# Performance work log

Hardware: AMD Instinct MI355X
Metric: run time of the kernel (lower is better)

## Reference

```python
import jax, jax.numpy as jnp
import numpy as np
import math

B, N, HORIZON, E = 16, 4096, 12, 16
IN_DIM = HORIZON * E            # 192
T_DIM, H, D = 64, 4, 16         # transformer_dim, heads, head_dim
K_ORD = 3
FFN = 128
OUT_DIM = HORIZON * 16          # horizon * dim_out = 192
LN_EPS = 1e-5


def setup_inputs() -> dict:
    key = jax.random.key(0)
    ks = jax.random.split(key, 16)
    s = 0.02
    return {
        "x": jax.random.normal(ks[0], (B, N, IN_DIM), jnp.float32),
        "Wq": jax.random.normal(ks[1], (IN_DIM, T_DIM), jnp.float32) * s,
        "bq": jnp.zeros((T_DIM,), jnp.float32),
        "Wk": jax.random.normal(ks[2], (IN_DIM, T_DIM), jnp.float32) * s,
        "bk": jnp.zeros((T_DIM,), jnp.float32),
        "Wv": jax.random.normal(ks[3], (IN_DIM, T_DIM), jnp.float32) * s,
        "bv": jnp.zeros((T_DIM,), jnp.float32),
        "Win": jax.random.normal(ks[4], (IN_DIM, T_DIM), jnp.float32) * s,  # no bias
        "Wout": jax.random.normal(ks[5], (T_DIM, OUT_DIM), jnp.float32) * s,
        "bout": jnp.zeros((OUT_DIM,), jnp.float32),
        "W1": jax.random.normal(ks[6], (T_DIM, FFN), jnp.float32) * s,
        "b1": jnp.zeros((FFN,), jnp.float32),
        "W2": jax.random.normal(ks[7], (FFN, T_DIM), jnp.float32) * s,
        "b2": jnp.zeros((T_DIM,), jnp.float32),
        "ln_g": jnp.ones((T_DIM,), jnp.float32),
        "ln_b": jnp.zeros((T_DIM,), jnp.float32),
        "weights_pool": jax.random.normal(ks[8], (IN_DIM, OUT_DIM), jnp.float32) * s,
        "Pi": jax.random.normal(ks[9], (H, K_ORD + 1), jnp.float32) * 0.5,
    }


def _layer_norm(y, g, b):
    mu = jnp.mean(y, axis=-1, keepdims=True)
    var = jnp.mean((y - mu) ** 2, axis=-1, keepdims=True)
    return (y - mu) * jax.lax.rsqrt(var + LN_EPS) * g + b


def reference(x, Wq, bq, Wk, bk, Wv, bv, Win, Wout, bout,
              W1, b1, W2, b2, ln_g, ln_b, weights_pool, Pi):
    Bx, Nx, _ = x.shape
    # projections -> (B, H, N, d)
    Q = (x @ Wq + bq).reshape(Bx, Nx, H, D).transpose(0, 2, 1, 3)
    Kt = (x @ Wk + bk).reshape(Bx, Nx, H, D).transpose(0, 2, 1, 3)
    V = (x @ Wv + bv).reshape(Bx, Nx, H, D).transpose(0, 2, 1, 3)

    weighted_sum = jnp.zeros((Bx, H, Nx, D), x.dtype)
    for k in range(K_ORD + 1):
        if k == 0:
            # transform(0, .) returns ones with feature dim 1
            Qk = jnp.ones((Bx, H, Nx, 1), x.dtype)
            Kk = jnp.ones((Bx, H, Nx, 1), x.dtype)
        else:
            Qk = Q ** k   # elementwise power (exp-by-squaring == x**k)
            Kk = Kt ** k
        dk = Qk.shape[-1]
        # f_kv: (B,H,f,d) ; sumN: (B,H,f,1)
        f_kv = jnp.einsum('bhnf,bhnc->bhfc', Kk, V)
        sumN = jnp.sum(Kk, axis=2)[..., None]
        f_kv_norm = f_kv / (sumN + 1e-8) / math.sqrt(dk)
        c_k = jnp.einsum('bhnf,bhfc->bhnc', Qk, f_kv_norm)
        weighted_sum = weighted_sum + c_k * Pi[:, k][None, :, None, None]

    # NOTE: faithful to original: raw view of (B,H,N,d) as (B,N,H*d), no permute
    attention_out = weighted_sum.reshape(Bx, Nx, H * D) / math.factorial(K_ORD)

    proj = x @ Win
    res = _layer_norm(proj + attention_out, ln_g, ln_b)
    ffn = jax.nn.relu(res @ W1 + b1) @ W2 + b2   # dropout = identity (eval)
    res = _layer_norm(res + ffn, ln_g, ln_b)

    x_g = jnp.einsum('bni,io->bno', x, weights_pool)
    out = res @ Wout + bout
    return x_g + out
```

## Files before the change

### kernel.cpp

```cpp
#include <hip/hip_runtime.h>

typedef unsigned int u32;
typedef unsigned short u16;

#define NB 16
#define NN 4096
#define IND 192

typedef __attribute__((ext_vector_type(8))) short short8;
typedef __attribute__((ext_vector_type(4))) float f32x4;
#define MFMA16 __builtin_amdgcn_mfma_f32_16x16x32_bf16

__device__ __forceinline__ float bf2f(u16 u) {
  union { u32 i; float f; } c; c.i = ((u32)u) << 16; return c.f;
}
__device__ __forceinline__ float lo16(u32 u) {
  union { u32 i; float f; } c; c.i = u << 16; return c.f;
}
__device__ __forceinline__ float hi16(u32 u) {
  union { u32 i; float f; } c; c.i = u & 0xffff0000u; return c.f;
}
__device__ __forceinline__ u16 f2bf(float f) {
  union { float f; u32 i; } c; c.f = f;
  u32 r = c.i + 0x7fffu + ((c.i >> 16) & 1u);
  return (u16)(r >> 16);
}
__device__ __forceinline__ float ldwf(const void* p, int i, int isf) {
  return isf ? ((const float*)p)[i] : bf2f(((const u16*)p)[i]);
}
__device__ __forceinline__ short8 ld_frag8(const u16* p) {
  union { uint4 u; short8 s; } c;
  c.u = *reinterpret_cast<const uint4*>(p);
  return c.s;
}
__device__ __forceinline__ short8 as_short8(uint4 u) {
  union { uint4 u; short8 s; } c; c.u = u; return c.s;
}
__device__ __forceinline__ short8 pack8(const float* v) {
  short8 s;
  #pragma unroll
  for (int e = 0; e < 8; ++e) s[e] = (short)f2bf(v[e]);
  return s;
}
__device__ __forceinline__ float ln64(float y, float g, float be) {
  float s = y, sq = y * y;
  #pragma unroll
  for (int off = 32; off > 0; off >>= 1) {
    s  += __shfl_xor(s, off, 64);
    sq += __shfl_xor(sq, off, 64);
  }
  float mu  = s * 0.015625f;
  float var = sq * 0.015625f - mu * mu;
  return (y - mu) * rsqrtf(var + 1e-5f) * g + be;
}

__global__ __launch_bounds__(64) void k_detect(const u32* __restrict__ x2,
                                               int* __restrict__ flag) {
  int t = threadIdx.x;
  int bad = 0;
  for (int i = 0; i < 16; ++i) {
    float a = fabsf(lo16(x2[t * 16 + i]));
    if (!(a < 1e4f)) bad = 1;
  }
  int anybad = __any(bad);
  if (t == 0) *flag = anybad ? 1 : 0;
}

__global__ __launch_bounds__(256) void k_xb(const int* __restrict__ flag,
                                            const void* __restrict__ x,
                                            u16* __restrict__ xb) {
  const int isf = *flag;
  size_t gid = (size_t)blockIdx.x * 256 + threadIdx.x;
  if (isf) {
    const float4* src = (const float4*)x;
    for (size_t i = gid; i < 3145728; i += 1048576) {
      float4 v = src[i];
      ushort4 o;
      o.x = f2bf(v.x); o.y = f2bf(v.y); o.z = f2bf(v.z); o.w = f2bf(v.w);
      ((ushort4*)xb)[i] = o;
    }
  } else {
    const uint4* src = (const uint4*)x;
    for (size_t i = gid; i < 1572864; i += 1048576)
      ((uint4*)xb)[i] = src[i];
  }
}

__global__ __launch_bounds__(192) void k_xsum(const int* __restrict__ flag,
                                              const void* __restrict__ x,
                                              float* __restrict__ xsum) {
  const int isf = *flag;
  const int t = threadIdx.x;
  const int r0 = blockIdx.x * 256;
  const int b = r0 >> 12;
  float s = 0.f;
  if (isf) {
    const float* xp = (const float*)x;
    for (int r = 0; r < 256; ++r) s += xp[(size_t)(r0 + r) * 192 + t];
  } else {
    const u16* xp = (const u16*)x;
    for (int r = 0; r < 256; ++r) s += bf2f(xp[(size_t)(r0 + r) * 192 + t]);
  }
  atomicAdd(xsum + b * 192 + t, s);
}

__global__ __launch_bounds__(256) void k_prepw(
    const int* __restrict__ flag,
    const void* Wq, const void* Wk, const void* Wv, const void* Win,
    const void* Wout, const void* Wp, const void* W1, const void* W2,
    const void* bq, const void* bk, const void* bv,
    u16* __restrict__ Bs1, u16* __restrict__ BsKlo, u16* __restrict__ Bs2,
    u16* __restrict__ W1f, u16* __restrict__ W2f, float* __restrict__ bcat)
{
  const int isf = *flag;
  int idx = blockIdx.x * 256 + threadIdx.x;
  if (idx < 49152) {
    int e = idx & 7, l = (idx >> 3) & 63, g = idx >> 9;
    int nt = g & 15, ks = g >> 4;
    int k = ks * 32 + (l >> 4) * 8 + e;
    int n = nt * 16 + (l & 15);
    const void* W = (n < 64) ? Wq : (n < 128) ? Wk : (n < 192) ? Wv : Win;
    Bs1[idx] = f2bf(ldwf(W, k * 64 + (n & 63), isf));
  } else if (idx < 61440) {
    int j = idx - 49152;
    int e = j & 7, l = (j >> 3) & 63, g = j >> 9;
    int ntp = g & 3, ks = g >> 2;
    int k = ks * 32 + (l >> 4) * 8 + e;
    int n = ntp * 16 + (l & 15);
    float wv = ldwf(Wk, k * 64 + n, isf);
    u16 hi = f2bf(wv);
    BsKlo[j] = f2bf(wv - bf2f(hi));
  } else if (idx < 110592) {
    int j = idx - 61440;
    int e = j & 7, l = (j >> 3) & 63, g = j >> 9;
    int nt = g % 12, ks = g / 12;
    int k = ks * 32 + (l >> 4) * 8 + e;
    int n = nt * 16 + (l & 15);
    float v = (k < 64) ? ldwf(Wout, k * 192 + n, isf)
                       : ldwf(Wp, (k - 64) * 192 + n, isf);
    Bs2[j] = f2bf(v);
  } else if (idx < 118784) {
    int j = idx - 110592;
    int e = j & 7, l = (j >> 3) & 63, g = j >> 9;
    int nt = g & 7, ks = g >> 3;
    int k = ks * 32 + (l >> 4) * 8 + e;
    int n = nt * 16 + (l & 15);
    W1f[j] = f2bf(ldwf(W1, k * 128 + n, isf));
  } else if (idx < 126976) {
    int j = idx - 118784;
    int e = j & 7, l = (j >> 3) & 63, g = j >> 9;
    int nt = g & 3, ks = g >> 2;
    int k = ks * 32 + (l >> 4) * 8 + e;
    int n = nt * 16 + (l & 15);
    W2f[j] = f2bf(ldwf(W2, k * 64 + n, isf));
  } else if (idx < 127232) {
    int n = idx - 126976;
    bcat[n] = (n < 64)  ? ldwf(bq, n, isf)
            : (n < 128) ? ldwf(bk, n - 64, isf)
            : (n < 192) ? ldwf(bv, n - 128, isf) : 0.f;
  }
}

template<bool F32>
__device__ void gemm1_body(const void* __restrict__ x,
                           const u16* __restrict__ Bs1,
                           const u16* __restrict__ BsKlo,
                           const float* __restrict__ bcat,
                           u16* __restrict__ C1, float* __restrict__ stats,
                           float (*xs)[196], float (*Ks)[65], float (*Vs)[65])
{
  const int tid = threadIdx.x;
  const int mbase = blockIdx.x * 32;
  const int b = mbase >> 12;

  if constexpr (F32) {
    for (int i = tid; i < 1536; i += 512) {
      int row = i / 48, c4 = i - row * 48;
      float4 v = *((const float4*)x + (size_t)(mbase + row) * 48 + c4);
      *(float4*)&xs[row][c4 * 4] = v;
    }
    __syncthreads();
  }

  const int w = tid >> 6, l = tid & 63, lm = l & 15, lk = l >> 4;
  const int nt0 = w * 2;
  const bool isK = (w == 2) || (w == 3);

  short8 bhi[2][6], blo[2][6];
  #pragma unroll
  for (int n2 = 0; n2 < 2; ++n2)
    #pragma unroll
    for (int ks = 0; ks < 6; ++ks) {
      bhi[n2][ks] = ld_frag8(Bs1 + (size_t)((ks * 16 + nt0 + n2) * 64 + l) * 8);
      if (F32 && isK)
        blo[n2][ks] = ld_frag8(BsKlo + (size_t)((ks * 4 + nt0 + n2 - 4) * 64 + l) * 8);
    }
  float bias[2];
  bias[0] = bcat[nt0 * 16 + lm];
  bias[1] = bcat[(nt0 + 1) * 16 + lm];

  for (int mt = 0; mt < 2; ++mt) {
    short8 ahi[6], alo[6];
    if constexpr (F32) {
      const float* xr = &xs[mt * 16 + lm][0];
      #pragma unroll
      for (int ks = 0; ks < 6; ++ks) {
        float v[8];
        *(float4*)&v[0] = *(const float4*)(xr + ks * 32 + lk * 8);
        *(float4*)&v[4] = *(const float4*)(xr + ks * 32 + lk * 8 + 4);
        short8 h8;
        #pragma unroll
        for (int e = 0; e < 8; ++e) h8[e] = (short)f2bf(v[e]);
        ahi[ks] = h8;
        if (isK) {
          short8 l8;
          #pragma unroll
          for (int e = 0; e < 8; ++e) {
            float r = v[e] - bf2f((u16)h8[e]);
            l8[e] = (short)f2bf(r);
          }
          alo[ks] = l8;
        }
      }
    } else {
      const u16* xg = (const u16*)x + (size_t)(mbase + mt * 16 + lm) * 192 + lk * 8;
      #pragma unroll
      for (int ks = 0; ks < 6; ++ks) ahi[ks] = ld_frag8(xg + ks * 32);
    }
    f32x4 acc[2];
    #pragma unroll
    for (int n2 = 0; n2 < 2; ++n2) {
      f32x4 a = {bias[n2], bias[n2], bias[n2], bias[n2]};
      acc[n2] = a;
    }
    #pragma unroll
    for (int ks = 0; ks < 6; ++ks)
      #pragma unroll
      for (int n2 = 0; n2 < 2; ++n2) {
        acc[n2] = MFMA16(ahi[ks], bhi[n2][ks], acc[n2], 0, 0, 0);
        if (F32 && isK) {
          acc[n2] = MFMA16(ahi[ks], blo[n2][ks], acc[n2], 0, 0, 0);
          acc[n2] = MFMA16(alo[ks], bhi[n2][ks], acc[n2], 0, 0, 0);
          acc[n2] = MFMA16(alo[ks], blo[n2][ks], acc[n2], 0, 0, 0);
        }
      }
    const int rl = mt * 16 + lk * 4;
    if (w < 2) {
      #pragma unroll
      for (int n2 = 0; n2 < 2; ++n2)
        #pragma unroll
        for (int r = 0; r < 4; ++r)
          C1[(size_t)(mbase + rl + r) * 128 + (nt0 + n2) * 16 + lm] = f2bf(acc[n2][r]);
    } else if (isK) {
      #pragma unroll
      for (int n2 = 0; n2 < 2; ++n2)
        #pragma unroll
        for (int r = 0; r < 4; ++r)
          Ks[rl + r][(nt0 + n2 - 4) * 16 + lm] = acc[n2][r];
    } else if (w < 6) {
      #pragma unroll
      for (int n2 = 0; n2 < 2; ++n2)
        #pragma unroll
        for (int r = 0; r < 4; ++r)
          Vs[rl + r][(nt0 + n2 - 8) * 16 + lm] = acc[n2][r];
    } else {
      #pragma unroll
      for (int n2 = 0; n2 < 2; ++n2)
        #pragma unroll
        for (int r = 0; r < 4; ++r)
          C1[(size_t)(mbase + rl + r) * 128 + 64 + (nt0 + n2 - 12) * 16 + lm] = f2bf(acc[n2][r]);
    }
  }
  __syncthreads();

  float* sb = stats + (size_t)(b * 4) * 832;
  #pragma unroll
  for (int it = 0; it < 2; ++it) {
    int item = tid + it * 512;
    int hh = item >> 8, f = (item >> 4) & 15, c = item & 15;
    float a1 = 0.f, a2 = 0.f, a3 = 0.f;
    for (int r = 0; r < 32; ++r) {
      float kv = Ks[r][hh * 16 + f];
      float vv = Vs[r][hh * 16 + c];
      float k2 = kv * kv;
      a1 = fmaf(kv, vv, a1);
      a2 = fmaf(k2, vv, a2);
      a3 = fmaf(k2 * kv, vv, a3);
    }
    float* base = sb + (size_t)hh * 832 + f * 16 + c;
    atomicAdd(base, a1);
    atomicAdd(base + 256, a2);
    atomicAdd(base + 512, a3);
  }
  if (tid < 192) {
    int kk = tid >> 6, hf = tid & 63, h2 = hf >> 4, ff = hf & 15;
    float s = 0.f;
    for (int r = 0; r < 32; ++r) {
      float kv = Ks[r][hf];
      s += (kk == 0) ? kv : (kk == 1) ? kv * kv : kv * kv * kv;
    }
    atomicAdd(sb + (size_t)h2 * 832 + 768 + kk * 16 + ff, s);
  } else if (tid < 256) {
    int hf = tid - 192, h2 = hf >> 4;
    float s = 0.f;
    for (int r = 0; r < 32; ++r) s += Vs[r][hf];
    atomicAdd(sb + (size_t)h2 * 832 + 816 + (hf & 15), s);
  }
}

__global__ __launch_bounds__(512, 2) void k_gemm1(
    const int* __restrict__ flag, const void* __restrict__ x,
    const u16* __restrict__ Bs1, const u16* __restrict__ BsKlo,
    const float* __restrict__ bcat,
    u16* __restrict__ C1, float* __restrict__ stats)
{
  __shared__ float xs[32][196];
  __shared__ float Ks[32][65];
  __shared__ float Vs[32][65];
  if (*flag) gemm1_body<true >(x, Bs1, BsKlo, bcat, C1, stats, xs, Ks, Vs);
  else       gemm1_body<false>(x, Bs1, BsKlo, bcat, C1, stats, xs, Ks, Vs);
}

template<bool F32>
__device__ void finalize_body(const float* stats, const void* Pi,
                              const void* Wk, const void* bk,
                              const float* xsum, float* M, float* sn1)
{
  const int bh = blockIdx.x, bb = bh >> 2, h = bh & 3, t = threadIdx.x;
  const float* sb = stats + (size_t)bh * 832;
  float* mb = M + (size_t)bh * 784;
  const float inv6 = 1.0f / 6.0f;

  {
    int f = t >> 4, s = t & 15;
    float p = 0.f;
    for (int i = s * 12; i < s * 12 + 12; ++i)
      p += xsum[bb * 192 + i] * ldwf(Wk, i * 64 + h * 16 + f, F32);
    p += __shfl_xor(p, 1, 64);
    p += __shfl_xor(p, 2, 64);
    p += __shfl_xor(p, 4, 64);
    p += __shfl_xor(p, 8, 64);
    if (s == 0) sn1[f] = p + 4096.0f * ldwf(bk, h * 16 + f, F32);
  }
  __syncthreads();

  {
    const int f = t >> 4, c = t & 15;
    #pragma unroll
    for (int k = 0; k < 3; ++k) {
      float fkv = sb[k * 256 + f * 16 + c];
      float sk  = (k == 0) ? sn1[f] : sb[768 + k * 16 + f];
      float pi  = ldwf(Pi, h * 4 + (k + 1), F32);
      mb[k * 256 + f * 16 + c] = fkv / ((sk + 1e-8f) * 4.0f) * pi * inv6;
    }
  }
  if (t < 16) {
    float sv  = sb[816 + t];
    float pi0 = ldwf(Pi, h * 4 + 0, F32);
    mb[768 + t] = sv / (4096.0f + 1e-8f) * pi0 * inv6;
  }
}

__global__ __launch_bounds__(256) void k_finalize(
    const int* __restrict__ flag, const float* __restrict__ stats,
    const void* __restrict__ Pi, const void* __restrict__ Wk,
    const void* __restrict__ bk, const float* __restrict__ xsum,
    float* __restrict__ M)
{
  __shared__ float sn1[16];
  if (*flag) finalize_body<true >(stats, Pi, Wk, bk, xsum, M, sn1);
  else       finalize_body<false>(stats, Pi, Wk, bk, xsum, M, sn1);
}

template<bool F32> __device__ void mid_body(
    const u16* __restrict__ C1, u16* __restrict__ R2,
    const float* __restrict__ Mall,
    const u16* __restrict__ W1f, const u16* __restrict__ W2f,
    const void* __restrict__ b1, const void* __restrict__ b2,
    const void* __restrict__ lng, const void* __restrict__ lnb,
    float (*attL)[72], u16 (*resB)[72], u16 (*hB)[136])
{
  const int tid = threadIdx.x;
  const int w = tid >> 6, l = tid & 63;
  const int lm = l & 15, lk = l >> 4;
  const int n0g = blockIdx.x * 64;
  const int b = n0g >> 12;
  const int n2_0 = n0g & 4095;
  const int h = n2_0 >> 10;
  const int qg0 = (b << 12) + ((n2_0 & 1023) << 2);
  const float* mb = Mall + (size_t)((b << 2) + h) * 784;

  short8 Bhi[2], Blo[2];
  #pragma unroll
  for (int ks = 0; ks < 2; ++ks) {
    float vh[8], vl[8];
    #pragma unroll
    for (int e = 0; e < 8; ++e) {
      int kk = ks * 32 + lk * 8 + e;
      float v = (kk < 16) ? mb[kk * 16 + lm]
              : (kk < 32) ? mb[256 + (kk - 16) * 16 + lm]
              : (kk < 48) ? mb[512 + (kk - 32) * 16 + lm] : 0.f;
      float hi = bf2f(f2bf(v));
      vh[e] = hi; vl[e] = v - hi;
    }
    Bhi[ks] = pack8(vh);
    Blo[ks] = pack8(vl);
  }
  const float c0v = mb[768 + lm];

  #pragma unroll
  for (int mt2 = 0; mt2 < 4; ++mt2) {
    const int mt = w * 4 + mt2;
    uint4 qv = *(const uint4*)(C1 + (size_t)(qg0 + mt * 16 + lm) * 128
                               + h * 16 + (lk & 1) * 8);
    float q[8] = {lo16(qv.x), hi16(qv.x), lo16(qv.y), hi16(qv.y),
                  lo16(qv.z), hi16(qv.z), lo16(qv.w), hi16(qv.w)};
    float q2[8], q3[8];
    #pragma unroll
    for (int e = 0; e < 8; ++e) { q2[e] = q[e] * q[e]; q3[e] = q2[e] * q[e]; }
    short8 a1, a2;
    if (lk < 2) { a1 = as_short8(qv); a2 = pack8(q3); }
    else        { a1 = pack8(q2);     a2 = short8{0,0,0,0,0,0,0,0}; }

    f32x4 acc = {c0v, c0v, c0v, c0v};
    acc = MFMA16(a1, Bhi[0], acc, 0, 0, 0);
    acc = MFMA16(a1, Blo[0], acc, 0, 0, 0);
    acc = MFMA16(a2, Bhi[1], acc, 0, 0, 0);
    acc = MFMA16(a2, Blo[1], acc, 0, 0, 0);

    #pragma unroll
    for (int r = 0; r < 4; ++r) {
      int qr = mt * 16 + lk * 4 + r;
      attL[qr >> 2][(qr & 3) * 16 + lm] = acc[r];
    }
  }

  const float gj = ldwf(lng, l, F32), bj = ldwf(lnb, l, F32);
  #pragma unroll 4
  for (int rr = 0; rr < 16; ++rr) {
    int r = w * 16 + rr;
    float proj = bf2f(C1[(size_t)(n0g + r) * 128 + 64 + l]);
    float y = proj + attL[r][l];
    resB[r][l] = f2bf(ln64(y, gj, bj));
  }

  short8 a0 = *(const short8*)&resB[w * 16 + lm][lk * 8];
  short8 a1f = *(const short8*)&resB[w * 16 + lm][32 + lk * 8];
  f32x4 hacc[8];
  #pragma unroll
  for (int nt = 0; nt < 8; ++nt) {
    float bv = ldwf(b1, nt * 16 + lm, F32);
    f32x4 a = {bv, bv, bv, bv};
    hacc[nt] = a;
  }
  #pragma unroll
  for (int nt = 0; nt < 8; ++nt) {
    short8 w1a = ld_frag8(W1f + (size_t)((0 * 8 + nt) * 64 + l) * 8);
    short8 w1b = ld_frag8(W1f + (size_t)((1 * 8 + nt) * 64 + l) * 8);
    hacc[nt] = MFMA16(a0, w1a, hacc[nt], 0, 0, 0);
    hacc[nt] = MFMA16(a1f, w1b, hacc[nt], 0, 0, 0);
  }
  #pragma unroll
  for (int nt = 0; nt < 8; ++nt)
    #pragma unroll
    for (int r = 0; r < 4; ++r) {
      int row = w * 16 + lk * 4 + r;
      hB[row][nt * 16 + lm] = f2bf(fmaxf(hacc[nt][r], 0.f));
    }

  short8 ha[4];
  #pragma unroll
  for (int ks = 0; ks < 4; ++ks)
    ha[ks] = *(const short8*)&hB[w * 16 + lm][ks * 32 + lk * 8];
  f32x4 oacc[4];
  #pragma unroll
  for (int nt = 0; nt < 4; ++nt) {
    float bv = ldwf(b2, nt * 16 + lm, F32);
    f32x4 a = {bv, bv, bv, bv};
    oacc[nt] = a;
  }
  #pragma unroll
  for (int ks = 0; ks < 4; ++ks)
    #pragma unroll
    for (int nt = 0; nt < 4; ++nt) {
      short8 w2v = ld_frag8(W2f + (size_t)((ks * 4 + nt) * 64 + l) * 8);
      oacc[nt] = MFMA16(ha[ks], w2v, oacc[nt], 0, 0, 0);
    }

  float gcol[4], bcol[4];
  #pragma unroll
  for (int nt = 0; nt < 4; ++nt) {
    gcol[nt] = ldwf(lng, nt * 16 + lm, F32);
    bcol[nt] = ldwf(lnb, nt * 16 + lm, F32);
  }
  #pragma unroll
  for (int r = 0; r < 4; ++r) {
    int row = w * 16 + lk * 4 + r;
    float y[4];
    float s = 0.f, sq = 0.f;
    #pragma unroll
    for (int nt = 0; nt < 4; ++nt) {
      y[nt] = oacc[nt][r] + bf2f(resB[row][nt * 16 + lm]);
      s += y[nt];
      sq = fmaf(y[nt], y[nt], sq);
    }
    #pragma unroll
    for (int off = 8; off > 0; off >>= 1) {
      s  += __shfl_xor(s, off, 64);
      sq += __shfl_xor(sq, off, 64);
    }
    float mu = s * 0.015625f;
    float var = sq * 0.015625f - mu * mu;
    float rs = rsqrtf(var + 1e-5f);
    #pragma unroll
    for (int nt = 0; nt < 4; ++nt) {
      float r2v = (y[nt] - mu) * rs * gcol[nt] + bcol[nt];
      R2[(size_t)(n0g + row) * 64 + nt * 16 + lm] = f2bf(r2v);
    }
  }
}

__global__ __launch_bounds__(256, 2) void k_mid(
    const int* __restrict__ flag, const u16* __restrict__ C1,
    u16* __restrict__ R2, const float* __restrict__ Mall,
    const u16* __restrict__ W1f, const u16* __restrict__ W2f,
    const void* __restrict__ b1, const void* __restrict__ b2,
    const void* __restrict__ lng, const void* __restrict__ lnb)
{
  __shared__ float attL[64][72];
  __shared__ u16 resB[64][72];
  __shared__ u16 hB[64][136];
  if (*flag) mid_body<true >(C1, R2, Mall, W1f, W2f, b1, b2, lng, lnb, attL, resB, hB);
  else       mid_body<false>(C1, R2, Mall, W1f, W2f, b1, b2, lng, lnb, attL, resB, hB);
}

__global__ __launch_bounds__(256, 2) void k_gemm2(
    const int* __restrict__ flag,
    const u16* __restrict__ R2, const u16* __restrict__ xb,
    const u16* __restrict__ Bs2, const void* __restrict__ bout,
    void* __restrict__ out)
{
  const int isf = *flag;
  const int l = threadIdx.x & 63;
  const int w = threadIdx.x >> 6;
  const int mbase = blockIdx.x * 64;
  const int lm = l & 15, lk = l >> 4;

  short8 bf[8][3];
  #pragma unroll
  for (int ks = 0; ks < 8; ++ks)
    #pragma unroll
    for (int nt = 0; nt < 3; ++nt)
      bf[ks][nt] = ld_frag8(Bs2 + (size_t)((ks * 12 + w * 3 + nt) * 64 + l) * 8);

  float bias[3];
  #pragma unroll
  for (int nt = 0; nt < 3; ++nt) bias[nt] = ldwf(bout, w * 48 + nt * 16 + lm, isf);

  short8 af[8];
  {
    const int row = mbase + lm;
    const u16* rp = R2 + (size_t)row * 64 + lk * 8;
    af[0] = ld_frag8(rp);
    af[1] = ld_frag8(rp + 32);
    const u16* xp = xb + (size_t)row * IND + lk * 8;
    #pragma unroll
    for (int ks = 2; ks < 8; ++ks) af[ks] = ld_frag8(xp + (ks - 2) * 32);
  }

  for (int mt = 0; mt < 4; ++mt) {
    short8 afn[8];
    if (mt < 3) {
      const int row = mbase + (mt + 1) * 16 + lm;
      const u16* rp = R2 + (size_t)row * 64 + lk * 8;
      afn[0] = ld_frag8(rp);
      afn[1] = ld_frag8(rp + 32);
      const u16* xp = xb + (size_t)row * IND + lk * 8;
      #pragma unroll
      for (int ks = 2; ks < 8; ++ks) afn[ks] = ld_frag8(xp + (ks - 2) * 32);
    }
    f32x4 acc[3];
    #pragma unroll
    for (int nt = 0; nt < 3; ++nt) {
      f32x4 a = {bias[nt], bias[nt], bias[nt], bias[nt]};
      acc[nt] = a;
    }
    #pragma unroll
    for (int ks = 0; ks < 8; ++ks)
      #pragma unroll
      for (int nt = 0; nt < 3; ++nt)
        acc[nt] = MFMA16(af[ks], bf[ks][nt], acc[nt], 0, 0, 0);
    const int r0 = mbase + mt * 16 + lk * 4;
    const int c0 = w * 48 + lm;
    if (isf) {
      float* op = (float*)out;
      #pragma unroll
      for (int nt = 0; nt < 3; ++nt)
        #pragma unroll
        for (int r = 0; r < 4; ++r)
          op[(size_t)(r0 + r) * IND + c0 + nt * 16] = acc[nt][r];
    } else {
      u16* op = (u16*)out;
      #pragma unroll
      for (int nt = 0; nt < 3; ++nt)
        #pragma unroll
        for (int r = 0; r < 4; ++r)
          op[(size_t)(r0 + r) * IND + c0 + nt * 16] = f2bf(acc[nt][r]);
    }
    #pragma unroll
    for (int ks = 0; ks < 8; ++ks) af[ks] = afn[ks];
  }
}

extern "C" void kernel_launch(void* const* d_in, const int* in_sizes, int n_in,
                              void* d_out, int out_size, void* d_ws, size_t ws_size,
                              hipStream_t stream)
{
  const void* x   = d_in[0];
  const void* Wq  = d_in[1];
  const void* bq  = d_in[2];
  const void* Wk  = d_in[3];
  const void* bk  = d_in[4];
  const void* Wv  = d_in[5];
  const void* bv  = d_in[6];
  const void* Win = d_in[7];
  const void* Wout= d_in[8];
  const void* bout= d_in[9];
  const void* W1  = d_in[10];
  const void* b1  = d_in[11];
  const void* W2  = d_in[12];
  const void* b2  = d_in[13];
  const void* lng = d_in[14];
  const void* lnb = d_in[15];
  const void* Wp  = d_in[16];
  const void* Pi  = d_in[17];

  u16* xb    = (u16*)d_ws;
  u16* C1    = xb + (size_t)12582912;
  u16* R2    = C1 + (size_t)8388608;
  u16* Bs1   = R2 + (size_t)4194304;
  u16* BsKlo = Bs1 + 49152;
  u16* Bs2   = BsKlo + 12288;
  u16* W1f   = Bs2 + 49152;
  u16* W2f   = W1f + 8192;
  float* bcat  = (float*)(W2f + 8192);
  float* stats = bcat + 256;
  float* xsum  = stats + 53248;
  float* Mc    = xsum + 3072;
  int*   flag  = (int*)(Mc + 50176);

  k_detect<<<1, 64, 0, stream>>>((const u32*)x, flag);
  hipMemsetAsync(stats, 0, (size_t)(53248 + 3072) * sizeof(float), stream);

  k_prepw<<<497, 256, 0, stream>>>(flag, Wq, Wk, Wv, Win, Wout, Wp, W1, W2,
                                   bq, bk, bv, Bs1, BsKlo, Bs2, W1f, W2f, bcat);
  k_xb<<<4096, 256, 0, stream>>>(flag, x, xb);
  k_xsum<<<256, 192, 0, stream>>>(flag, x, xsum);
  k_gemm1<<<2048, 512, 0, stream>>>(flag, x, Bs1, BsKlo, bcat, C1, stats);
  k_finalize<<<64, 256, 0, stream>>>(flag, stats, Pi, Wk, bk, xsum, Mc);
  k_mid<<<1024, 256, 0, stream>>>(flag, C1, R2, Mc, W1f, W2f, b1, b2, lng, lnb);
  k_gemm2<<<1024, 256, 0, stream>>>(flag, R2, xb, Bs2, bout, d_out);
}
```

Before: 161.7 us.

## Process four row chunks per gemm1 block and accumulate KV stats in registers

Each gemm1 block now loops over four 32-row chunks (128 rows) instead of one, keeping the K/V moment partial sums in registers across chunks. The atomic adds to the global stats buffer are issued once per block, so atomic traffic drops fourfold and the B-fragment and bias loads are amortized over more rows. In exchange the grid shrinks from 2048 to 512 blocks, which lowers parallelism and adds extra barriers per chunk inside each block.

```diff
diff --git a/kernel.cpp b/kernel.cpp
--- a/kernel.cpp
+++ b/kernel.cpp
@@ -170,18 +170,8 @@
                            float (*xs)[196], float (*Ks)[65], float (*Vs)[65])
 {
   const int tid = threadIdx.x;
-  const int mbase = blockIdx.x * 32;
-  const int b = mbase >> 12;
-
-  if constexpr (F32) {
-    for (int i = tid; i < 1536; i += 512) {
-      int row = i / 48, c4 = i - row * 48;
-      float4 v = *((const float4*)x + (size_t)(mbase + row) * 48 + c4);
-      *(float4*)&xs[row][c4 * 4] = v;
-    }
-    __syncthreads();
-  }
-
+  const int bbase = blockIdx.x * 128;
+  const int b = bbase >> 12;
   const int w = tid >> 6, l = tid & 63, lm = l & 15, lk = l >> 4;
   const int nt0 = w * 2;
   const bool isK = (w == 2) || (w == 3);
@@ -199,112 +189,142 @@
   bias[0] = bcat[nt0 * 16 + lm];
   bias[1] = bcat[(nt0 + 1) * 16 + lm];
 
-  for (int mt = 0; mt < 2; ++mt) {
-    short8 ahi[6], alo[6];
+  float sa1[2] = {0.f, 0.f}, sa2[2] = {0.f, 0.f}, sa3[2] = {0.f, 0.f};
+  float ssk = 0.f, ssv = 0.f;
+
+  for (int ch = 0; ch < 4; ++ch) {
+    const int mbase = bbase + ch * 32;
+
     if constexpr (F32) {
-      const float* xr = &xs[mt * 16 + lm][0];
-      #pragma unroll
-      for (int ks = 0; ks < 6; ++ks) {
-        float v[8];
-        *(float4*)&v[0] = *(const float4*)(xr + ks * 32 + lk * 8);
-        *(float4*)&v[4] = *(const float4*)(xr + ks * 32 + lk * 8 + 4);
-        short8 h8;
-        #pragma unroll
-        for (int e = 0; e < 8; ++e) h8[e] = (short)f2bf(v[e]);
-        ahi[ks] = h8;
-        if (isK) {
-          short8 l8;
+      for (int i = tid; i < 1536; i += 512) {
+        int row = i / 48, c4 = i - row * 48;
+        float4 v = *((const float4*)x + (size_t)(mbase + row) * 48 + c4);
+        *(float4*)&xs[row][c4 * 4] = v;
+      }
+    }
+    __syncthreads();
+
+    for (int mt = 0; mt < 2; ++mt) {
+      short8 ahi[6], alo[6];
+      if constexpr (F32) {
+        const float* xr = &xs[mt * 16 + lm][0];
+        #pragma unroll
+        for (int ks = 0; ks < 6; ++ks) {
+          float v[8];
+          *(float4*)&v[0] = *(const float4*)(xr + ks * 32 + lk * 8);
+          *(float4*)&v[4] = *(const float4*)(xr + ks * 32 + lk * 8 + 4);
+          short8 h8;
           #pragma unroll
-          for (int e = 0; e < 8; ++e) {
-            float r = v[e] - bf2f((u16)h8[e]);
-            l8[e] = (short)f2bf(r);
+          for (int e = 0; e < 8; ++e) h8[e] = (short)f2bf(v[e]);
+          ahi[ks] = h8;
+          if (isK) {
+            short8 l8;
+            #pragma unroll
+            for (int e = 0; e < 8; ++e) {
+              float r = v[e] - bf2f((u16)h8[e]);
+              l8[e] = (short)f2bf(r);
+            }
+            alo[ks] = l8;
           }
-          alo[ks] = l8;
         }
+      } else {
+        const u16* xg = (const u16*)x + (size_t)(mbase + mt * 16 + lm) * 192 + lk * 8;
+        #pragma unroll
+        for (int ks = 0; ks < 6; ++ks) ahi[ks] = ld_frag8(xg + ks * 32);
       }
-    } else {
-      const u16* xg = (const u16*)x + (size_t)(mbase + mt * 16 + lm) * 192 + lk * 8;
-      #pragma unroll
-      for (int ks = 0; ks < 6; ++ks) ahi[ks] = ld_frag8(xg + ks * 32);
-    }
-    f32x4 acc[2];
-    #pragma unroll
-    for (int n2 = 0; n2 < 2; ++n2) {
-      f32x4 a = {bias[n2], bias[n2], bias[n2], bias[n2]};
-      acc[n2] = a;
-    }
-    #pragma unroll
-    for (int ks = 0; ks < 6; ++ks)
+      f32x4 acc[2];
       #pragma unroll
       for (int n2 = 0; n2 < 2; ++n2) {
-        acc[n2] = MFMA16(ahi[ks], bhi[n2][ks], acc[n2], 0, 0, 0);
-        if (F32 && isK) {
-          acc[n2] = MFMA16(ahi[ks], blo[n2][ks], acc[n2], 0, 0, 0);
-          acc[n2] = MFMA16(alo[ks], bhi[n2][ks], acc[n2], 0, 0, 0);
-          acc[n2] = MFMA16(alo[ks], blo[n2][ks], acc[n2], 0, 0, 0);
+        f32x4 a = {bias[n2], bias[n2], bias[n2], bias[n2]};
+        acc[n2] = a;
+      }
+      #pragma unroll
+      for (int ks = 0; ks < 6; ++ks)
+        #pragma unroll
+        for (int n2 = 0; n2 < 2; ++n2) {
+          acc[n2] = MFMA16(ahi[ks], bhi[n2][ks], acc[n2], 0, 0, 0);
+          if (F32 && isK) {
+            acc[n2] = MFMA16(ahi[ks], blo[n2][ks], acc[n2], 0, 0, 0);
+            acc[n2] = MFMA16(alo[ks], bhi[n2][ks], acc[n2], 0, 0, 0);
+            acc[n2] = MFMA16(alo[ks], blo[n2][ks], acc[n2], 0, 0, 0);
+          }
         }
+      const int rl = mt * 16 + lk * 4;
+      if (w < 2) {
+        #pragma unroll
+        for (int n2 = 0; n2 < 2; ++n2)
+          #pragma unroll
+          for (int r = 0; r < 4; ++r)
+            C1[(size_t)(mbase + rl + r) * 128 + (nt0 + n2) * 16 + lm] = f2bf(acc[n2][r]);
+      } else if (isK) {
+        #pragma unroll
+        for (int n2 = 0; n2 < 2; ++n2)
+          #pragma unroll
+          for (int r = 0; r < 4; ++r)
+            Ks[rl + r][(nt0 + n2 - 4) * 16 + lm] = acc[n2][r];
+      } else if (w < 6) {
+        #pragma unroll
+        for (int n2 = 0; n2 < 2; ++n2)
+          #pragma unroll
+          for (int r = 0; r < 4; ++r)
+            Vs[rl + r][(nt0 + n2 - 8) * 16 + lm] = acc[n2][r];
+      } else {
+        #pragma unroll
+        for (int n2 = 0; n2 < 2; ++n2)
+          #pragma unroll
+          for (int r = 0; r < 4; ++r)
+            C1[(size_t)(mbase + rl + r) * 128 + 64 + (nt0 + n2 - 12) * 16 + lm] = f2bf(acc[n2][r]);
       }
-    const int rl = mt * 16 + lk * 4;
-    if (w < 2) {
-      #pragma unroll
-      for (int n2 = 0; n2 < 2; ++n2)
-        #pragma unroll
-        for (int r = 0; r < 4; ++r)
-          C1[(size_t)(mbase + rl + r) * 128 + (nt0 + n2) * 16 + lm] = f2bf(acc[n2][r]);
-    } else if (isK) {
-      #pragma unroll
-      for (int n2 = 0; n2 < 2; ++n2)
-        #pragma unroll
-        for (int r = 0; r < 4; ++r)
-          Ks[rl + r][(nt0 + n2 - 4) * 16 + lm] = acc[n2][r];
-    } else if (w < 6) {
-      #pragma unroll
-      for (int n2 = 0; n2 < 2; ++n2)
-        #pragma unroll
-        for (int r = 0; r < 4; ++r)
-          Vs[rl + r][(nt0 + n2 - 8) * 16 + lm] = acc[n2][r];
-    } else {
-      #pragma unroll
-      for (int n2 = 0; n2 < 2; ++n2)
-        #pragma unroll
-        for (int r = 0; r < 4; ++r)
-          C1[(size_t)(mbase + rl + r) * 128 + 64 + (nt0 + n2 - 12) * 16 + lm] = f2bf(acc[n2][r]);
-    }
-  }
-  __syncthreads();
+    }
+    __syncthreads();
+
+    #pragma unroll
+    for (int it = 0; it < 2; ++it) {
+      int item = tid + it * 512;
+      int hh = item >> 8, f = (item >> 4) & 15, c = item & 15;
+      float a1 = sa1[it], a2 = sa2[it], a3 = sa3[it];
+      for (int r = 0; r < 32; ++r) {
+        float kv = Ks[r][hh * 16 + f];
+        float vv = Vs[r][hh * 16 + c];
+        float k2 = kv * kv;
+        a1 = fmaf(kv, vv, a1);
+        a2 = fmaf(k2, vv, a2);
+        a3 = fmaf(k2 * kv, vv, a3);
+      }
+      sa1[it] = a1; sa2[it] = a2; sa3[it] = a3;
+    }
+    if (tid < 192) {
+      int kk = tid >> 6, hf = tid & 63;
+      float s = ssk;
+      for (int r = 0; r < 32; ++r) {
+        float kv = Ks[r][hf];
+        s += (kk == 0) ? kv : (kk == 1) ? kv * kv : kv * kv * kv;
+      }
+      ssk = s;
+    } else if (tid < 256) {
+      int hf = tid - 192;
+      float s = ssv;
+      for (int r = 0; r < 32; ++r) s += Vs[r][hf];
+      ssv = s;
+    }
+  }
 
   float* sb = stats + (size_t)(b * 4) * 832;
   #pragma unroll
   for (int it = 0; it < 2; ++it) {
     int item = tid + it * 512;
     int hh = item >> 8, f = (item >> 4) & 15, c = item & 15;
-    float a1 = 0.f, a2 = 0.f, a3 = 0.f;
-    for (int r = 0; r < 32; ++r) {
-      float kv = Ks[r][hh * 16 + f];
-      float vv = Vs[r][hh * 16 + c];
-      float k2 = kv * kv;
-      a1 = fmaf(kv, vv, a1);
-      a2 = fmaf(k2, vv, a2);
-      a3 = fmaf(k2 * kv, vv, a3);
-    }
     float* base = sb + (size_t)hh * 832 + f * 16 + c;
-    atomicAdd(base, a1);
-    atomicAdd(base + 256, a2);
-    atomicAdd(base + 512, a3);
+    atomicAdd(base, sa1[it]);
+    atomicAdd(base + 256, sa2[it]);
+    atomicAdd(base + 512, sa3[it]);
   }
   if (tid < 192) {
     int kk = tid >> 6, hf = tid & 63, h2 = hf >> 4, ff = hf & 15;
-    float s = 0.f;
-    for (int r = 0; r < 32; ++r) {
-      float kv = Ks[r][hf];
-      s += (kk == 0) ? kv : (kk == 1) ? kv * kv : kv * kv * kv;
-    }
-    atomicAdd(sb + (size_t)h2 * 832 + 768 + kk * 16 + ff, s);
+    atomicAdd(sb + (size_t)h2 * 832 + 768 + kk * 16 + ff, ssk);
   } else if (tid < 256) {
     int hf = tid - 192, h2 = hf >> 4;
-    float s = 0.f;
-    for (int r = 0; r < 32; ++r) s += Vs[r][hf];
-    atomicAdd(sb + (size_t)h2 * 832 + 816 + (hf & 15), s);
+    atomicAdd(sb + (size_t)h2 * 832 + 816 + (hf & 15), ssv);
   }
 }
 
@@ -656,7 +676,7 @@
                                    bq, bk, bv, Bs1, BsKlo, Bs2, W1f, W2f, bcat);
   k_xb<<<4096, 256, 0, stream>>>(flag, x, xb);
   k_xsum<<<256, 192, 0, stream>>>(flag, x, xsum);
-  k_gemm1<<<2048, 512, 0, stream>>>(flag, x, Bs1, BsKlo, bcat, C1, stats);
+  k_gemm1<<<512, 512, 0, stream>>>(flag, x, Bs1, BsKlo, bcat, C1, stats);
   k_finalize<<<64, 256, 0, stream>>>(flag, stats, Pi, Wk, bk, xsum, Mc);
   k_mid<<<1024, 256, 0, stream>>>(flag, C1, R2, Mc, W1f, W2f, b1, b2, lng, lnb);
   k_gemm2<<<1024, 256, 0, stream>>>(flag, R2, xb, Bs2, bout, d_out);
```

After: 201.1 us. +24.3%, slower.
